# Optimization experiments

Hardware: AMD Instinct MI355X
Metric: run time of the kernel (lower is better)

## Reference

```python
import jax, jax.numpy as jnp
import numpy as np

B, F0, D = 4096, 39, 16
CROSS_LAYER_SIZE = (128, 128)


def _he_uniform(key, shape):
    fan_in = int(np.prod(shape[:-1]))
    limit = np.sqrt(6.0 / fan_in)
    return jax.random.uniform(key, shape, jnp.float32, -limit, limit)


def setup_inputs() -> dict:
    key = jax.random.key(0)
    k_x, k_f0, k_f1, k_w, k_b = jax.random.split(key, 5)
    x = jax.random.normal(k_x, (B, F0, D), dtype=jnp.float32)
    # field_nums with direct=False: [39, 128//2=64, 64]
    f0 = _he_uniform(k_f0, (F0 * F0, CROSS_LAYER_SIZE[0]))          # (1521, 128)
    f1 = _he_uniform(k_f1, (F0 * (CROSS_LAYER_SIZE[0] // 2), CROSS_LAYER_SIZE[1]))  # (2496, 128)
    out_dim = CROSS_LAYER_SIZE[0] // 2 + CROSS_LAYER_SIZE[1]        # 192
    dense_w = _he_uniform(k_w, (out_dim, 1))
    dense_b = jnp.zeros((1,), dtype=jnp.float32)
    return {"x": x, "f0": f0, "f1": f1, "dense_w": dense_w, "dense_b": dense_b}


def reference(x, f0, f1, dense_w, dense_b):
    # CIN forward (direct=False, use_bias=False, use_residual=False, relu)
    # x: (B, F0, D)
    filters = [f0, f1]
    n_layers = len(CROSS_LAYER_SIZE)
    h = x  # hidden state, (B, Fk, D)
    finals = []
    for idx, L in enumerate(CROSS_LAYER_SIZE):
        Fk = h.shape[1]
        # filter f_ has shape (F0*Fk, L) with i (field of x0) major, j (field of h) minor
        Wr = filters[idx].reshape(F0, Fk, L)
        # fused outer product + conv1d (kernel width 1 == matmul over i,j):
        # z[b, m, d] = sum_{i,j} x[b,i,d] * h[b,j,d] * W[i,j,m]
        z = jnp.einsum('bid,bjd,ijm->bmd', x, h, Wr)  # (B, L, D)
        z = jax.nn.relu(z)
        if idx != n_layers - 1:
            # split along feature-map axis: first half feeds next layer,
            # second half goes to output
            h = z[:, : L // 2, :]
            finals.append(z[:, L // 2:, :])
        else:
            finals.append(z)
    result = jnp.sum(jnp.concatenate(finals, axis=1), axis=-1)  # (B, 192)
    return result @ dense_w + dense_b  # (B, 1)
```

## Files before the change

### kernel.cpp

```cpp
#include <hip/hip_runtime.h>


typedef _Float16 h2    __attribute__((ext_vector_type(2)));
typedef _Float16 f16x8 __attribute__((ext_vector_type(8)));
typedef __attribute__((ext_vector_type(16))) float f32x16;

#define XBB 1160
#define L0C 30
#define NCH 110

__device__ __constant__ int IG0[L0C] = {0,0,0,0,0, 1,1,1,1,1, 2,2,2,2, 3,3,3,3, 4,4,4, 5,5,5, 6,6, 7,7, 8, 9};
__device__ __constant__ int JG0[L0C] = {0,1,2,3,4, 0,1,2,3,4, 1,2,3,4, 1,2,3,4, 2,3,4, 2,3,4, 3,4, 3,4, 4, 4};
#define IG0T(c) ((c)<5?0:(c)<10?1:(c)<14?2:(c)<18?3:(c)<21?4:(c)<24?5:(c)<26?6:(c)<28?7:(c)<29?8:9)
#define JG0T(c) ((c)<10?((c)%5):(c)<18?(((c)-10)%4+1):(c)<24?(((c)-18)%3+2):(c)<28?(((c)-24)%2+3):4)

__global__ __launch_bounds__(256)
void CIN_repack(const float* __restrict__ f0, const float* __restrict__ f1,
                uint4* __restrict__ ws)
{
    const int tid  = blockIdx.x * 256 + threadIdx.x;
    const int n    = tid & 127;
    const int slot = tid >> 7;
    const int half = slot & 1;
    const int kh   = (slot >> 1) & 1;
    const int ch   = slot >> 2;
    float v[8];
    if (ch < L0C) {
        const int ig = IG0[ch], jg = JG0[ch];
        const int i = ig * 4 + kh * 2 + half;
#pragma unroll
        for (int t = 0; t < 8; ++t) {
            const int j = jg * 8 + t;
            float val = 0.f;
            if (i < 39 && j < 39 && j >= i) {
                val = f0[(i * 39 + j) * 128 + n];
                if (j > i) val += f0[(j * 39 + i) * 128 + n];
            }
            v[t] = val;
        }
    } else {
        const int c1 = ch - L0C;
        const int jg = c1 / 5, ig = c1 - jg * 5;
        const int j = jg * 4 + kh * 2 + half;
#pragma unroll
        for (int t = 0; t < 8; ++t) {
            const int i = ig * 8 + t;
            v[t] = (i < 39) ? f1[(i * 64 + j) * 128 + n] : 0.f;
        }
    }
    union { h2 h[4]; uint4 q; } pk;
#pragma unroll
    for (int t = 0; t < 4; ++t)
        pk.h[t] = h2{(_Float16)v[2 * t], (_Float16)v[2 * t + 1]};
    const int lane = half * 32 + (n & 31);
    const int cg   = n >> 5;
    ws[ch * 512 + kh * 256 + cg * 64 + lane] = pk.q;
}

__global__ __launch_bounds__(256, 4)
void CIN_main(const float* __restrict__ x,
              const char* __restrict__ wsB,
              const float* __restrict__ dw,
              const float* __restrict__ db,
              float* __restrict__ out)
{
    __shared__ __align__(16) _Float16 xsH[4 * XBB];
    __shared__ __align__(4)  _Float16 hsH[4][64][18];
    __shared__ float dws[192];
    __shared__ float red[4][4];

    const int tid  = threadIdx.x;
    const int w    = tid >> 6;
    const int lane = tid & 63;
    const int half = lane >> 5;
    const int d    = lane & 15;
    const int bsel = (lane >> 4) & 1;
    const int col  = lane & 31;

    const char* wbase = wsB + lane * 16 + w * 1024 + 2048;
    f16x8 Bb[2][2];
    auto loadBg = [&](int ch, f16x8 (&B)[2]) {
        const char* p0 = wbase + (size_t)ch * 8192;
        B[0] = *(const f16x8*)(p0 - 2048);
        B[1] = *(const f16x8*)(p0 + 2048);
    };

    loadBg(0, Bb[0]);
    loadBg(1, Bb[1]);

    const float4* xg4 = (const float4*)(x + (size_t)blockIdx.x * 4 * 624);
    for (int e4 = tid; e4 < 624; e4 += 256) {
        float4 v = xg4[e4];
        int bb = e4 / 156, r = e4 - bb * 156;
        int i = r >> 2, d0 = (r & 3) * 4;
        _Float16* bp = xsH + bb * XBB + i;
        bp[(d0 + 0) * 72] = (_Float16)v.x; bp[(d0 + 1) * 72] = (_Float16)v.y;
        bp[(d0 + 2) * 72] = (_Float16)v.z; bp[(d0 + 3) * 72] = (_Float16)v.w;
    }
    if (tid < 64) { int bb = tid >> 4, dd = tid & 15; xsH[bb * XBB + dd * 72 + 39] = (_Float16)0.f; }
    if (tid < 192) dws[tid] = dw[tid];
    __syncthreads();

    h2 xv[2][20];
#pragma unroll
    for (int p = 0; p < 2; ++p) {
        const uint4* src = (const uint4*)(xsH + (p * 2 + bsel) * XBB + d * 72);
#pragma unroll
        for (int q5 = 0; q5 < 5; ++q5) {
            union { uint4 q; h2 h[4]; } u;
            u.q = src[q5];
#pragma unroll
            for (int t = 0; t < 4; ++t) xv[p][q5 * 4 + t] = u.h[t];
        }
    }

    f32x16 acc[2];
#pragma unroll
    for (int p = 0; p < 2; ++p)
#pragma unroll
        for (int r = 0; r < 16; ++r) acc[p][r] = 0.f;

    h2 xiv2[2][2];

#pragma unroll
    for (int c = 0; c < L0C; ++c) {
        const int ig = IG0T(c);
        const int jg = JG0T(c);
        if (c == 0 || ig != IG0T(c - 1 < 0 ? 0 : c - 1)) {
#pragma unroll
            for (int p = 0; p < 2; ++p)
#pragma unroll
                for (int kh = 0; kh < 2; ++kh) {
                    _Float16 s = xsH[(p * 2 + bsel) * XBB + d * 72 + ig * 4 + kh * 2 + half];
                    xiv2[p][kh] = h2{s, s};
                }
        }
#pragma unroll
        for (int p = 0; p < 2; ++p) {
            union { h2 h[4]; f16x8 v; } a0, a1;
#pragma unroll
            for (int q = 0; q < 4; ++q) {
                a0.h[q] = xiv2[p][0] * xv[p][jg * 4 + q];
                a1.h[q] = xiv2[p][1] * xv[p][jg * 4 + q];
            }
            acc[p] = __builtin_amdgcn_mfma_f32_32x32x16_f16(a0.v, Bb[c & 1][0], acc[p], 0, 0, 0);
            acc[p] = __builtin_amdgcn_mfma_f32_32x32x16_f16(a1.v, Bb[c & 1][1], acc[p], 0, 0, 0);
        }
        loadBg(c + 2, Bb[c & 1]);
    }

    float cs[4] = {0.f, 0.f, 0.f, 0.f};
    if (w < 2) {
#pragma unroll
        for (int p = 0; p < 2; ++p)
#pragma unroll
            for (int r = 0; r < 16; r += 2) {
                const int row = (r & 3) + 8 * (r >> 2) + 4 * half;
                h2 pr = h2{(_Float16)fmaxf(acc[p][r],     0.f),
                           (_Float16)fmaxf(acc[p][r + 1], 0.f)};
                *(h2*)&hsH[p * 2 + (row >> 4)][w * 32 + col][row & 15] = pr;
            }
    } else {
        const float dwv = dws[(w - 2) * 32 + col];
#pragma unroll
        for (int p = 0; p < 2; ++p)
#pragma unroll
            for (int r = 0; r < 16; ++r) {
                const int row = (r & 3) + 8 * (r >> 2) + 4 * half;
                cs[p * 2 + (row >> 4)] += fmaxf(acc[p][r], 0.f) * dwv;
            }
    }
#pragma unroll
    for (int p = 0; p < 2; ++p)
#pragma unroll
        for (int r = 0; r < 16; ++r) acc[p][r] = 0.f;
    __syncthreads();

#pragma unroll 1
    for (int o2 = 0; o2 < 8; ++o2) {
#pragma unroll
        for (int u = 0; u < 10; ++u) {
            const int ch = L0C + o2 * 10 + u;
            const int ig2 = u % 5;
            if (ig2 == 0) {
                const int jb = (o2 * 2 + u / 5) * 4;
#pragma unroll
                for (int p = 0; p < 2; ++p)
#pragma unroll
                    for (int kh = 0; kh < 2; ++kh) {
                        _Float16 s = hsH[p * 2 + bsel][jb + kh * 2 + half][d];
                        xiv2[p][kh] = h2{s, s};
                    }
            }
#pragma unroll
            for (int p = 0; p < 2; ++p) {
                union { h2 h[4]; f16x8 v; } a0, a1;
#pragma unroll
                for (int q = 0; q < 4; ++q) {
                    a0.h[q] = xiv2[p][0] * xv[p][ig2 * 4 + q];
                    a1.h[q] = xiv2[p][1] * xv[p][ig2 * 4 + q];
                }
                acc[p] = __builtin_amdgcn_mfma_f32_32x32x16_f16(a0.v, Bb[u & 1][0], acc[p], 0, 0, 0);
                acc[p] = __builtin_amdgcn_mfma_f32_32x32x16_f16(a1.v, Bb[u & 1][1], acc[p], 0, 0, 0);
            }
            int chn = ch + 2; if (chn > NCH - 1) chn = NCH - 1;
            loadBg(chn, Bb[u & 1]);
        }
    }

    {
        const float dwv = dws[64 + w * 32 + col];
#pragma unroll
        for (int p = 0; p < 2; ++p)
#pragma unroll
            for (int r = 0; r < 16; ++r) {
                const int row = (r & 3) + 8 * (r >> 2) + 4 * half;
                cs[p * 2 + (row >> 4)] += fmaxf(acc[p][r], 0.f) * dwv;
            }
    }
#pragma unroll
    for (int rr = 0; rr < 4; ++rr)
#pragma unroll
        for (int off = 32; off > 0; off >>= 1)
            cs[rr] += __shfl_xor(cs[rr], off, 64);
    if (lane == 0) {
#pragma unroll
        for (int rr = 0; rr < 4; ++rr) red[w][rr] = cs[rr];
    }
    __syncthreads();
    if (tid < 4)
        out[blockIdx.x * 4 + tid] = red[0][tid] + red[1][tid] + red[2][tid] + red[3][tid] + db[0];
}

extern "C" void kernel_launch(void* const* d_in, const int* in_sizes, int n_in,
                              void* d_out, int out_size, void* d_ws, size_t ws_size,
                              hipStream_t stream)
{
    const float* x  = (const float*)d_in[0];
    const float* f0 = (const float*)d_in[1];
    const float* f1 = (const float*)d_in[2];
    const float* dw = (const float*)d_in[3];
    const float* db = (const float*)d_in[4];
    float* out = (float*)d_out;

    CIN_repack<<<dim3(220), dim3(256), 0, stream>>>(f0, f1, (uint4*)d_ws);
    CIN_main<<<dim3(1024), dim3(256), 0, stream>>>(x, (const char*)d_ws, dw, db, out);
}
```

Measured before the change: 125.1 us.

## Remap MFMA rows to batch with per-block d-slices and atomic output reduction

```diff
diff --git a/kernel.cpp b/kernel.cpp
--- a/kernel.cpp
+++ b/kernel.cpp
@@ -5,7 +5,6 @@
 typedef _Float16 f16x8 __attribute__((ext_vector_type(8)));
 typedef __attribute__((ext_vector_type(16))) float f32x16;
 
-#define XBB 1160
 #define L0C 30
 #define NCH 110
 
@@ -57,179 +56,187 @@
     ws[ch * 512 + kh * 256 + cg * 64 + lane] = pk.q;
 }
 
-__global__ __launch_bounds__(256, 4)
+__global__ __launch_bounds__(256)
+void CIN_init(float* __restrict__ out, const float* __restrict__ db)
+{
+    const int i = blockIdx.x * 256 + threadIdx.x;
+    if (i < 4096) out[i] = db[0];
+}
+
+__global__ __launch_bounds__(256)
 void CIN_main(const float* __restrict__ x,
               const char* __restrict__ wsB,
               const float* __restrict__ dw,
-              const float* __restrict__ db,
               float* __restrict__ out)
 {
-    __shared__ __align__(16) _Float16 xsH[4 * XBB];
-    __shared__ __align__(4)  _Float16 hsH[4][64][18];
+    __shared__ __align__(16) _Float16 xst[32 * 136 + 8];
+    __shared__ __align__(4)  _Float16 hst[64 * 66];
     __shared__ float dws[192];
-    __shared__ float red[4][4];
-
-    const int tid  = threadIdx.x;
-    const int w    = tid >> 6;
-    const int lane = tid & 63;
-    const int half = lane >> 5;
-    const int d    = lane & 15;
-    const int bsel = (lane >> 4) & 1;
-    const int col  = lane & 31;
-
-    const char* wbase = wsB + lane * 16 + w * 1024 + 2048;
+    __shared__ float redst[4][32];
+
+    const int tid   = threadIdx.x;
+    const int wvq   = tid >> 6;
+    const int lane  = tid & 63;
+    const int half  = lane >> 5;
+    const int b     = lane & 31;
+    const int btile = blockIdx.x >> 3;
+    const int wd    = blockIdx.x & 7;
+    const int d0    = wd * 2;
+
+    const char* wbase = wsB + lane * 16 + wvq * 1024 + 2048;
     f16x8 Bb[2][2];
     auto loadBg = [&](int ch, f16x8 (&B)[2]) {
         const char* p0 = wbase + (size_t)ch * 8192;
         B[0] = *(const f16x8*)(p0 - 2048);
         B[1] = *(const f16x8*)(p0 + 2048);
     };
-
     loadBg(0, Bb[0]);
     loadBg(1, Bb[1]);
 
-    const float4* xg4 = (const float4*)(x + (size_t)blockIdx.x * 4 * 624);
-    for (int e4 = tid; e4 < 624; e4 += 256) {
-        float4 v = xg4[e4];
-        int bb = e4 / 156, r = e4 - bb * 156;
-        int i = r >> 2, d0 = (r & 3) * 4;
-        _Float16* bp = xsH + bb * XBB + i;
-        bp[(d0 + 0) * 72] = (_Float16)v.x; bp[(d0 + 1) * 72] = (_Float16)v.y;
-        bp[(d0 + 2) * 72] = (_Float16)v.z; bp[(d0 + 3) * 72] = (_Float16)v.w;
-    }
-    if (tid < 64) { int bb = tid >> 4, dd = tid & 15; xsH[bb * XBB + dd * 72 + 39] = (_Float16)0.f; }
+    const float* xb = x + (size_t)btile * 32 * 624 + d0;
+    for (int slot = tid; slot < 1280; slot += 256) {
+        const int bb = slot / 40, i = slot - bb * 40;
+        float2 v = make_float2(0.f, 0.f);
+        if (i < 39) v = *(const float2*)(xb + (size_t)bb * 624 + i * 16);
+        xst[bb * 136 + i]      = (_Float16)v.x;
+        xst[bb * 136 + 64 + i] = (_Float16)v.y;
+    }
     if (tid < 192) dws[tid] = dw[tid];
     __syncthreads();
 
-    h2 xv[2][20];
-#pragma unroll
-    for (int p = 0; p < 2; ++p) {
-        const uint4* src = (const uint4*)(xsH + (p * 2 + bsel) * XBB + d * 72);
+    h2 xw[2][20];
+#pragma unroll
+    for (int s = 0; s < 2; ++s) {
+        const _Float16* base = xst + b * 136 + s * 64;
 #pragma unroll
         for (int q5 = 0; q5 < 5; ++q5) {
-            union { uint4 q; h2 h[4]; } u;
-            u.q = src[q5];
-#pragma unroll
-            for (int t = 0; t < 4; ++t) xv[p][q5 * 4 + t] = u.h[t];
+            union { f16x8 v; h2 h[4]; } u;
+            u.v = *(const f16x8*)(base + q5 * 8);
+#pragma unroll
+            for (int q = 0; q < 4; ++q) xw[s][q5 * 4 + q] = u.h[q];
         }
     }
 
     f32x16 acc[2];
 #pragma unroll
-    for (int p = 0; p < 2; ++p)
-#pragma unroll
-        for (int r = 0; r < 16; ++r) acc[p][r] = 0.f;
-
-    h2 xiv2[2][2];
+    for (int s = 0; s < 2; ++s)
+#pragma unroll
+        for (int r = 0; r < 16; ++r) acc[s][r] = 0.f;
+
+    h2 sp2[2][2];
 
 #pragma unroll
     for (int c = 0; c < L0C; ++c) {
         const int ig = IG0T(c);
         const int jg = JG0T(c);
-        if (c == 0 || ig != IG0T(c - 1 < 0 ? 0 : c - 1)) {
-#pragma unroll
-            for (int p = 0; p < 2; ++p)
+        if (c == 0 || IG0T(c) != IG0T(c - 1)) {
+#pragma unroll
+            for (int s = 0; s < 2; ++s)
 #pragma unroll
                 for (int kh = 0; kh < 2; ++kh) {
-                    _Float16 s = xsH[(p * 2 + bsel) * XBB + d * 72 + ig * 4 + kh * 2 + half];
-                    xiv2[p][kh] = h2{s, s};
+                    const h2 pr = xw[s][ig * 2 + kh];
+                    const _Float16 vv = half ? pr.y : pr.x;
+                    sp2[s][kh] = h2{vv, vv};
                 }
         }
 #pragma unroll
-        for (int p = 0; p < 2; ++p) {
+        for (int s = 0; s < 2; ++s) {
             union { h2 h[4]; f16x8 v; } a0, a1;
 #pragma unroll
             for (int q = 0; q < 4; ++q) {
-                a0.h[q] = xiv2[p][0] * xv[p][jg * 4 + q];
-                a1.h[q] = xiv2[p][1] * xv[p][jg * 4 + q];
-            }
-            acc[p] = __builtin_amdgcn_mfma_f32_32x32x16_f16(a0.v, Bb[c & 1][0], acc[p], 0, 0, 0);
-            acc[p] = __builtin_amdgcn_mfma_f32_32x32x16_f16(a1.v, Bb[c & 1][1], acc[p], 0, 0, 0);
+                a0.h[q] = sp2[s][0] * xw[s][jg * 4 + q];
+                a1.h[q] = sp2[s][1] * xw[s][jg * 4 + q];
+            }
+            acc[s] = __builtin_amdgcn_mfma_f32_32x32x16_f16(a0.v, Bb[c & 1][0], acc[s], 0, 0, 0);
+            acc[s] = __builtin_amdgcn_mfma_f32_32x32x16_f16(a1.v, Bb[c & 1][1], acc[s], 0, 0, 0);
         }
         loadBg(c + 2, Bb[c & 1]);
     }
 
-    float cs[4] = {0.f, 0.f, 0.f, 0.f};
-    if (w < 2) {
-#pragma unroll
-        for (int p = 0; p < 2; ++p)
-#pragma unroll
-            for (int r = 0; r < 16; r += 2) {
-                const int row = (r & 3) + 8 * (r >> 2) + 4 * half;
-                h2 pr = h2{(_Float16)fmaxf(acc[p][r],     0.f),
-                           (_Float16)fmaxf(acc[p][r + 1], 0.f)};
-                *(h2*)&hsH[p * 2 + (row >> 4)][w * 32 + col][row & 15] = pr;
-            }
-    } else {
-        const float dwv = dws[(w - 2) * 32 + col];
-#pragma unroll
-        for (int p = 0; p < 2; ++p)
+    float cs[16];
+#pragma unroll
+    for (int r = 0; r < 16; ++r) cs[r] = 0.f;
+    if (wvq < 2) {
+#pragma unroll
+        for (int s = 0; s < 2; ++s)
 #pragma unroll
             for (int r = 0; r < 16; ++r) {
                 const int row = (r & 3) + 8 * (r >> 2) + 4 * half;
-                cs[p * 2 + (row >> 4)] += fmaxf(acc[p][r], 0.f) * dwv;
-            }
-    }
-#pragma unroll
-    for (int p = 0; p < 2; ++p)
-#pragma unroll
-        for (int r = 0; r < 16; ++r) acc[p][r] = 0.f;
+                hst[(wvq * 32 + b) * 66 + row * 2 + s] =
+                    (_Float16)fmaxf(acc[s][r], 0.f);
+            }
+    } else {
+        const float dwv = dws[(wvq - 2) * 32 + b];
+#pragma unroll
+        for (int s = 0; s < 2; ++s)
+#pragma unroll
+            for (int r = 0; r < 16; ++r)
+                cs[r] += fmaxf(acc[s][r], 0.f) * dwv;
+    }
+#pragma unroll
+    for (int s = 0; s < 2; ++s)
+#pragma unroll
+        for (int r = 0; r < 16; ++r) acc[s][r] = 0.f;
     __syncthreads();
 
 #pragma unroll 1
     for (int o2 = 0; o2 < 8; ++o2) {
 #pragma unroll
         for (int u = 0; u < 10; ++u) {
-            const int ch = L0C + o2 * 10 + u;
+            const int pos = o2 * 10 + u;
             const int ig2 = u % 5;
             if (ig2 == 0) {
                 const int jb = (o2 * 2 + u / 5) * 4;
 #pragma unroll
-                for (int p = 0; p < 2; ++p)
+                for (int s = 0; s < 2; ++s)
 #pragma unroll
                     for (int kh = 0; kh < 2; ++kh) {
-                        _Float16 s = hsH[p * 2 + bsel][jb + kh * 2 + half][d];
-                        xiv2[p][kh] = h2{s, s};
+                        const _Float16 vv = hst[(jb + kh * 2 + half) * 66 + b * 2 + s];
+                        sp2[s][kh] = h2{vv, vv};
                     }
             }
 #pragma unroll
-            for (int p = 0; p < 2; ++p) {
+            for (int s = 0; s < 2; ++s) {
                 union { h2 h[4]; f16x8 v; } a0, a1;
 #pragma unroll
                 for (int q = 0; q < 4; ++q) {
-                    a0.h[q] = xiv2[p][0] * xv[p][ig2 * 4 + q];
-                    a1.h[q] = xiv2[p][1] * xv[p][ig2 * 4 + q];
+                    a0.h[q] = sp2[s][0] * xw[s][ig2 * 4 + q];
+                    a1.h[q] = sp2[s][1] * xw[s][ig2 * 4 + q];
                 }
-                acc[p] = __builtin_amdgcn_mfma_f32_32x32x16_f16(a0.v, Bb[u & 1][0], acc[p], 0, 0, 0);
-                acc[p] = __builtin_amdgcn_mfma_f32_32x32x16_f16(a1.v, Bb[u & 1][1], acc[p], 0, 0, 0);
-            }
-            int chn = ch + 2; if (chn > NCH - 1) chn = NCH - 1;
-            loadBg(chn, Bb[u & 1]);
+                acc[s] = __builtin_amdgcn_mfma_f32_32x32x16_f16(a0.v, Bb[pos & 1][0], acc[s], 0, 0, 0);
+                acc[s] = __builtin_amdgcn_mfma_f32_32x32x16_f16(a1.v, Bb[pos & 1][1], acc[s], 0, 0, 0);
+            }
+            int chn = 30 + pos + 2; if (chn > NCH - 1) chn = NCH - 1;
+            loadBg(chn, Bb[pos & 1]);
         }
     }
 
     {
-        const float dwv = dws[64 + w * 32 + col];
-#pragma unroll
-        for (int p = 0; p < 2; ++p)
-#pragma unroll
-            for (int r = 0; r < 16; ++r) {
-                const int row = (r & 3) + 8 * (r >> 2) + 4 * half;
-                cs[p * 2 + (row >> 4)] += fmaxf(acc[p][r], 0.f) * dwv;
-            }
-    }
-#pragma unroll
-    for (int rr = 0; rr < 4; ++rr)
-#pragma unroll
-        for (int off = 32; off > 0; off >>= 1)
-            cs[rr] += __shfl_xor(cs[rr], off, 64);
-    if (lane == 0) {
-#pragma unroll
-        for (int rr = 0; rr < 4; ++rr) red[w][rr] = cs[rr];
+        const float dwv = dws[64 + wvq * 32 + b];
+#pragma unroll
+        for (int s = 0; s < 2; ++s)
+#pragma unroll
+            for (int r = 0; r < 16; ++r)
+                cs[r] += fmaxf(acc[s][r], 0.f) * dwv;
+    }
+
+#pragma unroll
+    for (int r = 0; r < 16; ++r)
+#pragma unroll
+        for (int off = 1; off < 32; off <<= 1)
+            cs[r] += __shfl_xor(cs[r], off, 64);
+    if ((lane & 31) == 0) {
+#pragma unroll
+        for (int r = 0; r < 16; ++r) {
+            const int row = (r & 3) + 8 * (r >> 2) + 4 * half;
+            redst[wvq][row] = cs[r];
+        }
     }
     __syncthreads();
-    if (tid < 4)
-        out[blockIdx.x * 4 + tid] = red[0][tid] + red[1][tid] + red[2][tid] + red[3][tid] + db[0];
+    if (tid < 32) {
+        const float v = redst[0][tid] + redst[1][tid] + redst[2][tid] + redst[3][tid];
+        atomicAdd(&out[btile * 32 + tid], v);
+    }
 }
 
 extern "C" void kernel_launch(void* const* d_in, const int* in_sizes, int n_in,
@@ -244,5 +251,6 @@
     float* out = (float*)d_out;
 
     CIN_repack<<<dim3(220), dim3(256), 0, stream>>>(f0, f1, (uint4*)d_ws);
-    CIN_main<<<dim3(1024), dim3(256), 0, stream>>>(x, (const char*)d_ws, dw, db, out);
-}
+    CIN_init<<<dim3(16), dim3(256), 0, stream>>>(out, db);
+    CIN_main<<<dim3(1024), dim3(256), 0, stream>>>(x, (const char*)d_ws, dw, out);
+}
```

Result: slower. 134.9 us (+7.8%).
